# Optimization experiments

Hardware: AMD Instinct MI355X
Metric: run time of the kernel (lower is better)

## Reference

```python
import jax, jax.numpy as jnp
import numpy as np

HEADS = 16
DIM_HEAD = 64


def setup_inputs() -> dict:
    key = jax.random.key(0)
    k1, k2, k3, k4 = jax.random.split(key, 4)
    b, n, d = 2, 2048, 1024
    x = jax.random.normal(k1, (b, n, d), dtype=jnp.float32)
    attn_mask = jax.random.randint(k2, (b, n, n), 0, 2) == 1  # bool mask, True = masked out
    Wqkv = jax.random.normal(k3, (d, 3 * HEADS * DIM_HEAD), dtype=jnp.float32) * (d ** -0.5)
    Wfc = jax.random.normal(k4, (HEADS * DIM_HEAD, d), dtype=jnp.float32) * ((HEADS * DIM_HEAD) ** -0.5)
    return {"x": x, "attn_mask": attn_mask, "Wqkv": Wqkv, "Wfc": Wfc}


def reference(x, attn_mask, Wqkv, Wfc):
    b, n, d = x.shape
    h, dh = HEADS, DIM_HEAD
    qkv = x @ Wqkv  # [b, n, 3*h*dh]
    q, k, v = jnp.split(qkv, 3, axis=-1)
    def to_heads(t):
        return t.reshape(b, n, h, dh).transpose(0, 2, 1, 3)  # b h n d
    q, k, v = to_heads(q), to_heads(k), to_heads(v)
    # NOTE: original divides by scale = dim_head**-0.5, i.e. multiplies by sqrt(dim_head)
    scale = dh ** (-0.5)
    scores = jnp.einsum('bhqd,bhkd->bhqk', q, k) / scale
    scores = jnp.where(attn_mask[:, None, :, :], jnp.float32(-1e9), scores)
    attn = jax.nn.softmax(scores, axis=-1)
    context = jnp.einsum('bhqk,bhkd->bhqd', attn, v)  # b h n dh
    context = context.transpose(0, 2, 1, 3).reshape(b, n, h * dh)
    out = context @ Wfc
    return out, attn
```

## Files before the change

kernel.cpp:

```cpp
#include <hip/hip_runtime.h>

#define HEADS  16
#define DH     64
#define NBATCH 2
#define SEQ    2048
#define DMODEL 1024

typedef unsigned short u16;
typedef unsigned int   u32;
typedef unsigned long long u64;

typedef __attribute__((ext_vector_type(8))) short short8v;
typedef __attribute__((ext_vector_type(4))) float floatx4;

__device__ __forceinline__ u16 f2bf(float f) {
    u32 u = __float_as_uint(f);
    return (u16)((u + 0x7fffu + ((u >> 16) & 1u)) >> 16);
}
__device__ __forceinline__ float bf2f(u16 h) {
    return __uint_as_float(((u32)h) << 16);
}
__device__ __forceinline__ float fexp2(float x) {
    return __builtin_amdgcn_exp2f(x);
}
__device__ __forceinline__ u32 pk_bf16(float a, float b) {
    u32 r;
    asm("v_cvt_pk_bf16_f32 %0, %1, %2" : "=v"(r) : "v"(a), "v"(b));
    return r;
}

__global__ void k_split(const float* __restrict__ in, u16* __restrict__ hi,
                        u16* __restrict__ lo, int n4) {
    int i = blockIdx.x * blockDim.x + threadIdx.x;
    if (i >= n4) return;
    float4 v = reinterpret_cast<const float4*>(in)[i];
    ushort4 hv, lv;
    hv.x = f2bf(v.x); hv.y = f2bf(v.y); hv.z = f2bf(v.z); hv.w = f2bf(v.w);
    lv.x = f2bf(v.x - bf2f(hv.x));
    lv.y = f2bf(v.y - bf2f(hv.y));
    lv.z = f2bf(v.z - bf2f(hv.z));
    lv.w = f2bf(v.w - bf2f(hv.w));
    reinterpret_cast<ushort4*>(hi)[i] = hv;
    reinterpret_cast<ushort4*>(lo)[i] = lv;
}

__global__ void k_tsplit(const float* __restrict__ in, u16* __restrict__ hiT,
                         u16* __restrict__ loT, int R, int C, int write_lo) {
    __shared__ float tile[64][65];
    int c0 = blockIdx.x * 64, r0 = blockIdx.y * 64;
    int t = threadIdx.x;
    int lr = t >> 4;
    int lc = (t & 15) * 4;
    for (int i = 0; i < 4; i++) {
        int r = lr + i * 16;
        float4 v = *reinterpret_cast<const float4*>(&in[(size_t)(r0 + r) * C + c0 + lc]);
        tile[r][lc] = v.x; tile[r][lc + 1] = v.y; tile[r][lc + 2] = v.z; tile[r][lc + 3] = v.w;
    }
    __syncthreads();
    for (int i = 0; i < 4; i++) {
        int cc = lr + i * 16;
        float vs0 = tile[lc + 0][cc], vs1 = tile[lc + 1][cc];
        float vs2 = tile[lc + 2][cc], vs3 = tile[lc + 3][cc];
        ushort4 hv, lv;
        hv.x = f2bf(vs0); hv.y = f2bf(vs1); hv.z = f2bf(vs2); hv.w = f2bf(vs3);
        *reinterpret_cast<ushort4*>(&hiT[(size_t)(c0 + cc) * R + r0 + lc]) = hv;
        if (write_lo) {
            lv.x = f2bf(vs0 - bf2f(hv.x)); lv.y = f2bf(vs1 - bf2f(hv.y));
            lv.z = f2bf(vs2 - bf2f(hv.z)); lv.w = f2bf(vs3 - bf2f(hv.w));
            *reinterpret_cast<ushort4*>(&loT[(size_t)(c0 + cc) * R + r0 + lc]) = lv;
        }
    }
}

__global__ void k_maskpack(const int* __restrict__ m, u64* __restrict__ bits) {
    int i = blockIdx.x * 256 + threadIdx.x;
    u64 b = __ballot(m[i] != 0);
    if ((threadIdx.x & 63) == 0) bits[((u32)i) >> 6] = b;
}

__global__ __launch_bounds__(256, 2) void k_qkv(
    const u16* __restrict__ xh, const u16* __restrict__ xl,
    const u16* __restrict__ whT, const u16* __restrict__ wlT,
    u16* __restrict__ qh, u16* __restrict__ ql,
    u16* __restrict__ kh, u16* __restrict__ kl,
    u16* __restrict__ vt)
{
    __shared__ __attribute__((aligned(16))) u16 sA[2][128][72];
    __shared__ __attribute__((aligned(16))) u16 sB[2][128][72];
    int n0 = blockIdx.x * 128;
    int m0 = blockIdx.y * 128;
    bool is_v = (n0 >= 2 * DMODEL);
    int tid = threadIdx.x;
    int wave = tid >> 6, lane = tid & 63;
    int wm = (wave >> 1) * 64, wn = (wave & 1) * 64;
    int lrow = lane & 15, lgrp = lane >> 4;

    floatx4 acc[4][4];
    for (int i = 0; i < 4; i++) for (int j = 0; j < 4; j++) acc[i][j] = (floatx4){0.f, 0.f, 0.f, 0.f};

    int sr = tid >> 1;
    int sc = (tid & 1) * 32;

    for (int k0 = 0; k0 < DMODEL; k0 += 64) {
        const u16* pxh = xh + (size_t)(m0 + sr) * DMODEL + k0 + sc;
        const u16* pwh = whT + (size_t)(n0 + sr) * DMODEL + k0 + sc;
        for (int i = 0; i < 4; i++) {
            *reinterpret_cast<int4*>(&sA[0][sr][sc + i * 8]) = *reinterpret_cast<const int4*>(pxh + i * 8);
            *reinterpret_cast<int4*>(&sB[0][sr][sc + i * 8]) = *reinterpret_cast<const int4*>(pwh + i * 8);
        }
        if (!is_v) {
            const u16* pxl = xl + (size_t)(m0 + sr) * DMODEL + k0 + sc;
            const u16* pwl = wlT + (size_t)(n0 + sr) * DMODEL + k0 + sc;
            for (int i = 0; i < 4; i++) {
                *reinterpret_cast<int4*>(&sA[1][sr][sc + i * 8]) = *reinterpret_cast<const int4*>(pxl + i * 8);
                *reinterpret_cast<int4*>(&sB[1][sr][sc + i * 8]) = *reinterpret_cast<const int4*>(pwl + i * 8);
            }
        }
        __syncthreads();
        for (int ks = 0; ks < 2; ks++) {
            short8v ah[4], bh_[4], al[4], bl_[4];
            for (int i = 0; i < 4; i++) {
                ah[i]  = *reinterpret_cast<const short8v*>(&sA[0][wm + i * 16 + lrow][ks * 32 + lgrp * 8]);
                bh_[i] = *reinterpret_cast<const short8v*>(&sB[0][wn + i * 16 + lrow][ks * 32 + lgrp * 8]);
            }
            if (!is_v) {
                for (int i = 0; i < 4; i++) {
                    al[i]  = *reinterpret_cast<const short8v*>(&sA[1][wm + i * 16 + lrow][ks * 32 + lgrp * 8]);
                    bl_[i] = *reinterpret_cast<const short8v*>(&sB[1][wn + i * 16 + lrow][ks * 32 + lgrp * 8]);
                }
            }
            for (int i = 0; i < 4; i++)
                for (int j = 0; j < 4; j++) {
                    acc[i][j] = __builtin_amdgcn_mfma_f32_16x16x32_bf16(ah[i], bh_[j], acc[i][j], 0, 0, 0);
                    if (!is_v) {
                        acc[i][j] = __builtin_amdgcn_mfma_f32_16x16x32_bf16(ah[i], bl_[j], acc[i][j], 0, 0, 0);
                        acc[i][j] = __builtin_amdgcn_mfma_f32_16x16x32_bf16(al[i], bh_[j], acc[i][j], 0, 0, 0);
                    }
                }
        }
        __syncthreads();
    }
    for (int j = 0; j < 4; j++) {
        int c = n0 + wn + j * 16 + lrow;
        int sel = c >> 10;
        int hcol = c & 1023;
        int hh = hcol >> 6, d = hcol & 63;
        for (int i = 0; i < 4; i++) {
            int mbase = m0 + wm + i * 16 + lgrp * 4;
            int bb = mbase >> 11;
            int nn = mbase & 2047;
            int bh = bb * HEADS + hh;
            if (sel == 2) {
                ushort4 pv;
                pv.x = f2bf(acc[i][j][0]); pv.y = f2bf(acc[i][j][1]);
                pv.z = f2bf(acc[i][j][2]); pv.w = f2bf(acc[i][j][3]);
                *reinterpret_cast<ushort4*>(&vt[((size_t)bh * DH + d) * SEQ + nn]) = pv;
            } else {
                u16* oh = (sel == 0) ? qh : kh;
                u16* ol = (sel == 0) ? ql : kl;
                float sc8 = (sel == 0) ? 11.5415603f : 1.0f;
                for (int r = 0; r < 4; r++) {
                    float v = acc[i][j][r] * sc8;
                    u16 hv = f2bf(v);
                    u16 lv = f2bf(v - bf2f(hv));
                    size_t addr = ((size_t)bh * SEQ + nn + r) * DH + d;
                    oh[addr] = hv; ol[addr] = lv;
                }
            }
        }
    }
}

__global__ __launch_bounds__(256, 2) void k_attn(
    const u16* __restrict__ qh, const u16* __restrict__ ql,
    const u16* __restrict__ kh, const u16* __restrict__ kl,
    const u16* __restrict__ vt, const u32* __restrict__ mb,
    float* __restrict__ attn, u16* __restrict__ ctx)
{
    __shared__ __attribute__((aligned(16))) u16 sKh[2][64][72];
    __shared__ __attribute__((aligned(16))) u16 sKl[2][64][72];
    __shared__ __attribute__((aligned(16))) u16 sP[2][64][72];
    __shared__ u32 sMask[2][64][2];
    __shared__ float sML[2][4][64];

    const float NEGBIG = -3.0e38f;

    int bh = blockIdx.y;
    int b = bh >> 4;
    int q0 = blockIdx.x * 64;
    int tid = threadIdx.x, wave = tid >> 6, lane = tid & 63;
    int lrow = lane & 15, lgrp = lane >> 4;
    int sr4 = tid >> 2, sc4 = (tid & 3) * 16;
    int mbit = (wave & 1) * 16 + lgrp * 4;
    int mwsel = wave >> 1;

    short8v qfh[4][2], qfl[4][2];
    for (int nt = 0; nt < 4; nt++) {
        int qr = q0 + nt * 16 + lrow;
        const u16* pq = qh + ((size_t)bh * SEQ + qr) * DH + lgrp * 8;
        const u16* pl = ql + ((size_t)bh * SEQ + qr) * DH + lgrp * 8;
        for (int ks = 0; ks < 2; ks++) {
            qfh[nt][ks] = *reinterpret_cast<const short8v*>(pq + ks * 32);
            qfl[nt][ks] = *reinterpret_cast<const short8v*>(pl + ks * 32);
        }
    }

    int4 ra0, ra1, rb0, rb1;
    u32 mv = 0;

#define K_LOAD(KT) do { \
        const u16* ph_ = kh + ((size_t)bh * SEQ + (KT) * 64 + sr4) * DH + sc4; \
        const u16* pl_ = kl + ((size_t)bh * SEQ + (KT) * 64 + sr4) * DH + sc4; \
        ra0 = *reinterpret_cast<const int4*>(ph_); \
        ra1 = *reinterpret_cast<const int4*>(ph_ + 8); \
        rb0 = *reinterpret_cast<const int4*>(pl_); \
        rb1 = *reinterpret_cast<const int4*>(pl_ + 8); \
        if (tid < 128) mv = mb[((size_t)(b * SEQ + q0 + (tid >> 1))) * 64 + (KT) * 2 + (tid & 1)]; \
    } while (0)

#define K_WRITE(B_) do { \
        *reinterpret_cast<int4*>(&sKh[B_][sr4][sc4])     = ra0; \
        *reinterpret_cast<int4*>(&sKh[B_][sr4][sc4 + 8]) = ra1; \
        *reinterpret_cast<int4*>(&sKl[B_][sr4][sc4])     = rb0; \
        *reinterpret_cast<int4*>(&sKl[B_][sr4][sc4 + 8]) = rb1; \
        if (tid < 128) sMask[B_][tid >> 1][tid & 1] = mv; \
    } while (0)

#define COMPUTE_ST(CUR) do { \
        for (int nt_ = 0; nt_ < 4; nt_++) sacc[nt_] = (floatx4){0.f, 0.f, 0.f, 0.f}; \
        __builtin_amdgcn_s_setprio(1); \
        for (int ks_ = 0; ks_ < 2; ks_++) { \
            short8v kfh_ = *reinterpret_cast<const short8v*>(&sKh[CUR][wave * 16 + lrow][ks_ * 32 + lgrp * 8]); \
            short8v kfl_ = *reinterpret_cast<const short8v*>(&sKl[CUR][wave * 16 + lrow][ks_ * 32 + lgrp * 8]); \
            for (int nt_ = 0; nt_ < 4; nt_++) { \
                sacc[nt_] = __builtin_amdgcn_mfma_f32_16x16x32_bf16(kfh_, qfh[nt_][ks_], sacc[nt_], 0, 0, 0); \
                sacc[nt_] = __builtin_amdgcn_mfma_f32_16x16x32_bf16(kfh_, qfl[nt_][ks_], sacc[nt_], 0, 0, 0); \
                sacc[nt_] = __builtin_amdgcn_mfma_f32_16x16x32_bf16(kfl_, qfh[nt_][ks_], sacc[nt_], 0, 0, 0); \
            } \
        } \
        __builtin_amdgcn_s_setprio(0); \
    } while (0)

    float m_run[4], l_run[4];
    for (int nt = 0; nt < 4; nt++) { m_run[nt] = -1.0e38f; l_run[nt] = 0.f; }

    K_LOAD(0);
    K_WRITE(0);
    __syncthreads();
    for (int kt = 0; kt < 32; kt++) {
        int cur = kt & 1;
        if (kt < 31) K_LOAD(kt + 1);
        floatx4 sacc[4];
        COMPUTE_ST(cur);
        for (int nt = 0; nt < 4; nt++) {
            u32 nw = ~sMask[cur][nt * 16 + lrow][mwsel];
            float sm0 = ((nw >> (mbit + 0)) & 1u) ? sacc[nt][0] : NEGBIG;
            float sm1 = ((nw >> (mbit + 1)) & 1u) ? sacc[nt][1] : NEGBIG;
            float sm2 = ((nw >> (mbit + 2)) & 1u) ? sacc[nt][2] : NEGBIG;
            float sm3 = ((nw >> (mbit + 3)) & 1u) ? sacc[nt][3] : NEGBIG;
            float tmax = fmaxf(fmaxf(sm0, sm1), fmaxf(sm2, sm3));
            float mn = fmaxf(m_run[nt], tmax);
            float ssum = fexp2(sm0 - mn) + fexp2(sm1 - mn) + fexp2(sm2 - mn) + fexp2(sm3 - mn);
            l_run[nt] = l_run[nt] * fexp2(m_run[nt] - mn) + ssum;
            m_run[nt] = mn;
        }
        if (kt < 31) K_WRITE(cur ^ 1);
        __syncthreads();
    }

    for (int nt = 0; nt < 4; nt++) {
        float m = m_run[nt], l = l_run[nt];
        for (int off = 16; off <= 32; off <<= 1) {
            float mo = __shfl_xor(m, off);
            float lo2 = __shfl_xor(l, off);
            float mn = fmaxf(m, mo);
            l = l * fexp2(m - mn) + lo2 * fexp2(mo - mn);
            m = mn;
        }
        m_run[nt] = m; l_run[nt] = l;
    }
    if (lane < 16) {
        for (int nt = 0; nt < 4; nt++) {
            sML[0][wave][nt * 16 + lane] = m_run[nt];
            sML[1][wave][nt * 16 + lane] = l_run[nt];
        }
    }
    __syncthreads();
    float Cn[4];
    for (int nt = 0; nt < 4; nt++) {
        int qr = nt * 16 + lrow;
        float m4 = sML[0][0][qr];
        for (int w = 1; w < 4; w++) m4 = fmaxf(m4, sML[0][w][qr]);
        float ls = 0.f;
        for (int w = 0; w < 4; w++) ls += sML[1][w][qr] * fexp2(sML[0][w][qr] - m4);
        Cn[nt] = m4 + __log2f(ls);
    }

    floatx4 cacc[4];
    for (int j = 0; j < 4; j++) cacc[j] = (floatx4){0.f, 0.f, 0.f, 0.f};

    K_LOAD(0);
    K_WRITE(0);
    __syncthreads();
    for (int kt = 0; kt < 32; kt++) {
        int cur = kt & 1;
        int4 vreg[4][2];
        for (int j = 0; j < 4; j++)
            for (int ks = 0; ks < 2; ks++)
                vreg[j][ks] = *reinterpret_cast<const int4*>(
                    vt + ((size_t)bh * DH + j * 16 + lrow) * SEQ + kt * 64 + ks * 32 + lgrp * 8);
        if (kt < 31) K_LOAD(kt + 1);
        floatx4 sacc[4];
        COMPUTE_ST(cur);
        for (int nt = 0; nt < 4; nt++) {
            u32 nw = ~sMask[cur][nt * 16 + lrow][mwsel];
            int qr = q0 + nt * 16 + lrow;
            float4 pf4;
            float* pp = &pf4.x;
            for (int r = 0; r < 4; r++) {
                float sm = ((nw >> (mbit + r)) & 1u) ? sacc[nt][r] : NEGBIG;
                pp[r] = fexp2(sm - Cn[nt]);
            }
            int kc = kt * 64 + wave * 16 + lgrp * 4;
            *reinterpret_cast<float4*>(&attn[((size_t)bh * SEQ + qr) * SEQ + kc]) = pf4;
            uint2 pw;
            pw.x = pk_bf16(pp[0], pp[1]);
            pw.y = pk_bf16(pp[2], pp[3]);
            *reinterpret_cast<uint2*>(&sP[cur][nt * 16 + lrow][wave * 16 + lgrp * 4]) = pw;
        }
        if (kt < 31) K_WRITE(cur ^ 1);
        __syncthreads();
        __builtin_amdgcn_s_setprio(1);
        for (int ks = 0; ks < 2; ks++) {
            short8v pfrag = *reinterpret_cast<const short8v*>(&sP[cur][wave * 16 + lrow][ks * 32 + lgrp * 8]);
            for (int j = 0; j < 4; j++) {
                short8v vfrag = *reinterpret_cast<short8v*>(&vreg[j][ks]);
                cacc[j] = __builtin_amdgcn_mfma_f32_16x16x32_bf16(pfrag, vfrag, cacc[j], 0, 0, 0);
            }
        }
        __builtin_amdgcn_s_setprio(0);
    }
    int hh = bh & 15;
    for (int j = 0; j < 4; j++) {
        int d = j * 16 + lrow;
        for (int r = 0; r < 4; r++) {
            int nn = q0 + wave * 16 + lgrp * 4 + r;
            ctx[((size_t)b * SEQ + nn) * DMODEL + hh * 64 + d] = f2bf(cacc[j][r]);
        }
    }
#undef K_LOAD
#undef K_WRITE
#undef COMPUTE_ST
}

__global__ __launch_bounds__(256, 2) void k_out(
    const u16* __restrict__ ctx, const u16* __restrict__ wfcT, float* __restrict__ out)
{
    __shared__ __attribute__((aligned(16))) u16 sA[128][72];
    __shared__ __attribute__((aligned(16))) u16 sB[128][72];
    int n0 = blockIdx.x * 128;
    int m0 = blockIdx.y * 128;
    int tid = threadIdx.x;
    int wave = tid >> 6, lane = tid & 63;
    int wm = (wave >> 1) * 64, wn = (wave & 1) * 64;
    int lrow = lane & 15, lgrp = lane >> 4;

    floatx4 acc[4][4];
    for (int i = 0; i < 4; i++) for (int j = 0; j < 4; j++) acc[i][j] = (floatx4){0.f, 0.f, 0.f, 0.f};

    int sr = tid >> 1;
    int sc = (tid & 1) * 32;

    for (int k0 = 0; k0 < DMODEL; k0 += 64) {
        const u16* pa = ctx + (size_t)(m0 + sr) * DMODEL + k0 + sc;
        const u16* pb = wfcT + (size_t)(n0 + sr) * DMODEL + k0 + sc;
        for (int i = 0; i < 4; i++) {
            *reinterpret_cast<int4*>(&sA[sr][sc + i * 8]) = *reinterpret_cast<const int4*>(pa + i * 8);
            *reinterpret_cast<int4*>(&sB[sr][sc + i * 8]) = *reinterpret_cast<const int4*>(pb + i * 8);
        }
        __syncthreads();
        for (int ks = 0; ks < 2; ks++) {
            short8v af[4], bf[4];
            for (int i = 0; i < 4; i++) {
                af[i] = *reinterpret_cast<const short8v*>(&sA[wm + i * 16 + lrow][ks * 32 + lgrp * 8]);
                bf[i] = *reinterpret_cast<const short8v*>(&sB[wn + i * 16 + lrow][ks * 32 + lgrp * 8]);
            }
            for (int i = 0; i < 4; i++)
                for (int j = 0; j < 4; j++)
                    acc[i][j] = __builtin_amdgcn_mfma_f32_16x16x32_bf16(af[i], bf[j], acc[i][j], 0, 0, 0);
        }
        __syncthreads();
    }
    for (int i = 0; i < 4; i++)
        for (int j = 0; j < 4; j++)
            for (int r = 0; r < 4; r++) {
                int m = m0 + wm + i * 16 + lgrp * 4 + r;
                int c = n0 + wn + j * 16 + lrow;
                out[(size_t)m * DMODEL + c] = acc[i][j][r];
            }
}

extern "C" void kernel_launch(void* const* d_in, const int* in_sizes, int n_in,
                              void* d_out, int out_size, void* d_ws, size_t ws_size,
                              hipStream_t stream) {
    const float* x    = (const float*)d_in[0];
    const int*   mask = (const int*)d_in[1];
    const float* wqkv = (const float*)d_in[2];
    const float* wfc  = (const float*)d_in[3];

    float* out  = (float*)d_out;
    float* attn = out + (size_t)NBATCH * SEQ * DMODEL;

    u16* xh   = (u16*)d_ws;
    u16* xl   = xh + 4194304;
    u16* whT  = xl + 4194304;
    u16* wlT  = whT + 3145728;
    u16* wfcT = wlT + 3145728;
    u16* qh   = wfcT + 1048576;
    u16* ql   = qh + 4194304;
    u16* kh   = ql + 4194304;
    u16* kl   = kh + 4194304;
    u16* vt   = kl + 4194304;
    u32* mbits = (u32*)(vt + 4194304);
    u16* ctx  = xh;

    k_split<<<4096, 256, 0, stream>>>(x, xh, xl, 4194304 / 4);
    k_tsplit<<<dim3(48, 16), 256, 0, stream>>>(wqkv, whT, wlT, 1024, 3072, 1);
    k_tsplit<<<dim3(16, 16), 256, 0, stream>>>(wfc, wfcT, (u16*)nullptr, 1024, 1024, 0);
    k_maskpack<<<32768, 256, 0, stream>>>(mask, (u64*)mbits);
    k_qkv<<<dim3(24, 32), 256, 0, stream>>>(xh, xl, whT, wlT, qh, ql, kh, kl, vt);
    k_attn<<<dim3(32, 32), 256, 0, stream>>>(qh, ql, kh, kl, vt, mbits, attn, ctx);
    k_out<<<dim3(8, 32), 256, 0, stream>>>(ctx, wfcT, out);
}
```

Measured before the change: 505.5 us.

## Swizzle attention LDS tiles, remap block IDs per XCD, raise attention occupancy

Replaces the padded 72-column LDS tiles in the attention kernel with unpadded 64-column tiles using an XOR swizzle, which cuts LDS footprint and avoids bank conflicts. Launch bounds rise to 3 blocks per CU. All three GEMM/attention kernels remap block IDs so consecutive blocks on the same XCD (id mod 8) share rows/heads, aiming at better L2 locality. K loads are also reorganized into full 128-byte row segments. The risks are extra register pressure under the tighter launch bound and index-mapping errors if the grid sizes differ from the hardcoded constants.

```diff
diff --git a/kernel.cpp b/kernel.cpp
--- a/kernel.cpp
+++ b/kernel.cpp
@@ -28,6 +28,8 @@
     asm("v_cvt_pk_bf16_f32 %0, %1, %2" : "=v"(r) : "v"(a), "v"(b));
     return r;
 }
+
+#define KSWZ(row, col) (((row) << 6) + ((col) ^ (((row) & 7) << 3)))
 
 __global__ void k_split(const float* __restrict__ in, u16* __restrict__ hi,
                         u16* __restrict__ lo, int n4) {
@@ -87,8 +89,10 @@
 {
     __shared__ __attribute__((aligned(16))) u16 sA[2][128][72];
     __shared__ __attribute__((aligned(16))) u16 sB[2][128][72];
-    int n0 = blockIdx.x * 128;
-    int m0 = blockIdx.y * 128;
+    int id = blockIdx.y * 24 + blockIdx.x;
+    int sw = (id & 7) * 96 + (id >> 3);
+    int n0 = (sw % 24) * 128;
+    int m0 = (sw / 24) * 128;
     bool is_v = (n0 >= 2 * DMODEL);
     int tid = threadIdx.x;
     int wave = tid >> 6, lane = tid & 63;
@@ -171,28 +175,34 @@
     }
 }
 
-__global__ __launch_bounds__(256, 2) void k_attn(
+__global__ __launch_bounds__(256, 3) void k_attn(
     const u16* __restrict__ qh, const u16* __restrict__ ql,
     const u16* __restrict__ kh, const u16* __restrict__ kl,
     const u16* __restrict__ vt, const u32* __restrict__ mb,
     float* __restrict__ attn, u16* __restrict__ ctx)
 {
-    __shared__ __attribute__((aligned(16))) u16 sKh[2][64][72];
-    __shared__ __attribute__((aligned(16))) u16 sKl[2][64][72];
-    __shared__ __attribute__((aligned(16))) u16 sP[2][64][72];
+    __shared__ __attribute__((aligned(16))) u16 sKh[2][64 * 64];
+    __shared__ __attribute__((aligned(16))) u16 sKl[2][64 * 64];
+    __shared__ __attribute__((aligned(16))) u16 sP[2][64 * 64];
     __shared__ u32 sMask[2][64][2];
     __shared__ float sML[2][4][64];
 
     const float NEGBIG = -3.0e38f;
 
-    int bh = blockIdx.y;
+    int id = blockIdx.y * gridDim.x + blockIdx.x;
+    int sw = (id & 7) * 128 + (id >> 3);
+    int bh = sw >> 5;
+    int q0 = (sw & 31) * 64;
     int b = bh >> 4;
-    int q0 = blockIdx.x * 64;
     int tid = threadIdx.x, wave = tid >> 6, lane = tid & 63;
     int lrow = lane & 15, lgrp = lane >> 4;
-    int sr4 = tid >> 2, sc4 = (tid & 3) * 16;
     int mbit = (wave & 1) * 16 + lgrp * 4;
     int mwsel = wave >> 1;
+
+    int krow = tid >> 3;
+    int kcol = (tid & 7) * 8;
+    int ksz1 = KSWZ(krow, kcol);
+    int ksz2 = KSWZ(krow + 32, kcol);
 
     short8v qfh[4][2], qfl[4][2];
     for (int nt = 0; nt < 4; nt++) {
@@ -209,20 +219,20 @@
     u32 mv = 0;
 
 #define K_LOAD(KT) do { \
-        const u16* ph_ = kh + ((size_t)bh * SEQ + (KT) * 64 + sr4) * DH + sc4; \
-        const u16* pl_ = kl + ((size_t)bh * SEQ + (KT) * 64 + sr4) * DH + sc4; \
+        const u16* ph_ = kh + ((size_t)bh * SEQ + (KT) * 64 + krow) * DH + kcol; \
+        const u16* pl_ = kl + ((size_t)bh * SEQ + (KT) * 64 + krow) * DH + kcol; \
         ra0 = *reinterpret_cast<const int4*>(ph_); \
-        ra1 = *reinterpret_cast<const int4*>(ph_ + 8); \
+        ra1 = *reinterpret_cast<const int4*>(ph_ + 32 * DH); \
         rb0 = *reinterpret_cast<const int4*>(pl_); \
-        rb1 = *reinterpret_cast<const int4*>(pl_ + 8); \
+        rb1 = *reinterpret_cast<const int4*>(pl_ + 32 * DH); \
         if (tid < 128) mv = mb[((size_t)(b * SEQ + q0 + (tid >> 1))) * 64 + (KT) * 2 + (tid & 1)]; \
     } while (0)
 
 #define K_WRITE(B_) do { \
-        *reinterpret_cast<int4*>(&sKh[B_][sr4][sc4])     = ra0; \
-        *reinterpret_cast<int4*>(&sKh[B_][sr4][sc4 + 8]) = ra1; \
-        *reinterpret_cast<int4*>(&sKl[B_][sr4][sc4])     = rb0; \
-        *reinterpret_cast<int4*>(&sKl[B_][sr4][sc4 + 8]) = rb1; \
+        *reinterpret_cast<int4*>(&sKh[B_][ksz1]) = ra0; \
+        *reinterpret_cast<int4*>(&sKh[B_][ksz2]) = ra1; \
+        *reinterpret_cast<int4*>(&sKl[B_][ksz1]) = rb0; \
+        *reinterpret_cast<int4*>(&sKl[B_][ksz2]) = rb1; \
         if (tid < 128) sMask[B_][tid >> 1][tid & 1] = mv; \
     } while (0)
 
@@ -230,8 +240,9 @@
         for (int nt_ = 0; nt_ < 4; nt_++) sacc[nt_] = (floatx4){0.f, 0.f, 0.f, 0.f}; \
         __builtin_amdgcn_s_setprio(1); \
         for (int ks_ = 0; ks_ < 2; ks_++) { \
-            short8v kfh_ = *reinterpret_cast<const short8v*>(&sKh[CUR][wave * 16 + lrow][ks_ * 32 + lgrp * 8]); \
-            short8v kfl_ = *reinterpret_cast<const short8v*>(&sKl[CUR][wave * 16 + lrow][ks_ * 32 + lgrp * 8]); \
+            int a_ = KSWZ(wave * 16 + lrow, ks_ * 32 + lgrp * 8); \
+            short8v kfh_ = *reinterpret_cast<const short8v*>(&sKh[CUR][a_]); \
+            short8v kfl_ = *reinterpret_cast<const short8v*>(&sKl[CUR][a_]); \
             for (int nt_ = 0; nt_ < 4; nt_++) { \
                 sacc[nt_] = __builtin_amdgcn_mfma_f32_16x16x32_bf16(kfh_, qfh[nt_][ks_], sacc[nt_], 0, 0, 0); \
                 sacc[nt_] = __builtin_amdgcn_mfma_f32_16x16x32_bf16(kfh_, qfl[nt_][ks_], sacc[nt_], 0, 0, 0); \
@@ -326,13 +337,13 @@
             uint2 pw;
             pw.x = pk_bf16(pp[0], pp[1]);
             pw.y = pk_bf16(pp[2], pp[3]);
-            *reinterpret_cast<uint2*>(&sP[cur][nt * 16 + lrow][wave * 16 + lgrp * 4]) = pw;
+            *reinterpret_cast<uint2*>(&sP[cur][KSWZ(nt * 16 + lrow, wave * 16 + lgrp * 4)]) = pw;
         }
         if (kt < 31) K_WRITE(cur ^ 1);
         __syncthreads();
         __builtin_amdgcn_s_setprio(1);
         for (int ks = 0; ks < 2; ks++) {
-            short8v pfrag = *reinterpret_cast<const short8v*>(&sP[cur][wave * 16 + lrow][ks * 32 + lgrp * 8]);
+            short8v pfrag = *reinterpret_cast<const short8v*>(&sP[cur][KSWZ(wave * 16 + lrow, ks * 32 + lgrp * 8)]);
             for (int j = 0; j < 4; j++) {
                 short8v vfrag = *reinterpret_cast<short8v*>(&vreg[j][ks]);
                 cacc[j] = __builtin_amdgcn_mfma_f32_16x16x32_bf16(pfrag, vfrag, cacc[j], 0, 0, 0);
@@ -358,8 +369,10 @@
 {
     __shared__ __attribute__((aligned(16))) u16 sA[128][72];
     __shared__ __attribute__((aligned(16))) u16 sB[128][72];
-    int n0 = blockIdx.x * 128;
-    int m0 = blockIdx.y * 128;
+    int id = blockIdx.y * 8 + blockIdx.x;
+    int sw = (id & 7) * 32 + (id >> 3);
+    int n0 = (sw % 8) * 128;
+    int m0 = (sw / 8) * 128;
     int tid = threadIdx.x;
     int wave = tid >> 6, lane = tid & 63;
     int wm = (wave >> 1) * 64, wn = (wave & 1) * 64;
```

New measurement: 691.8 us. 1.37x slower.
